# Kernel tuning notes

Hardware: AMD Instinct MI355X
Metric: run time of the kernel (lower is better)

Reference implementation:

```python
import jax, jax.numpy as jnp
import numpy as np

H, W, N = 1024, 2048, 1572864
NF, NP, NIN = 32, 3, 5


def _linear_init(key, fan_in, fan_out):
    kw, kb = jax.random.split(key)
    bound = 1.0 / np.sqrt(fan_in)
    w = jax.random.uniform(kw, (fan_in, fan_out), jnp.float32, -bound, bound)
    b = jax.random.uniform(kb, (fan_out,), jnp.float32, -bound, bound)
    return w, b


def setup_inputs() -> dict:
    key = jax.random.key(0)
    ks = jax.random.split(key, 8)
    # grid: sub-pixel source coordinates, (2, N), x-row then y-row
    gx = jax.random.uniform(ks[0], (1, N), jnp.float32) * (W - 1)
    gy = jax.random.uniform(ks[1], (1, N), jnp.float32) * (H - 1)
    grid = jnp.concatenate([gx, gy], axis=0)
    # yi: unique flat pixel indices (torch index-assign assumes no duplicates)
    yi = jax.random.permutation(ks[2], H * W)[:N].astype(jnp.int32)
    # m: near-identity homography so the projective denominator stays well-conditioned
    m = jnp.eye(3, dtype=jnp.float32) + 0.05 * jax.random.normal(ks[3], (3, 3), jnp.float32)
    W1, b1 = _linear_init(ks[4], NIN, NF)
    W2, b2 = _linear_init(ks[5], NF, NF)
    W3, b3 = _linear_init(ks[6], NF, NF)
    W4, b4 = _linear_init(ks[7], NF, NP)
    return {"grid": grid, "yi": yi, "m": m,
            "W1": W1, "b1": b1, "W2": W2, "b2": b2,
            "W3": W3, "b3": b3, "W4": W4, "b4": b4,
            "size_h": H, "size_w": W}


def _calc_dsda_projective(m, h, w):
    # Area scale (Jacobian determinant magnitude) of the homography m at each
    # output pixel: |det(m)| / |m20*x + m21*y + m22|^3, flattened row-major (H*W,)
    xs = jnp.arange(w, dtype=jnp.float32)
    ys = jnp.arange(h, dtype=jnp.float32)
    denom = m[2, 0] * xs[None, :] + m[2, 1] * ys[:, None] + m[2, 2]  # (H, W)
    det = jnp.linalg.det(m)
    return (jnp.abs(det) / (jnp.abs(denom) ** 3)).reshape(-1)


def reference(grid, yi, m, W1, b1, W2, b2, W3, b3, W4, b4, size_h, size_w):
    h, w = size_h, size_w
    # --- feature construction (torch.no_grad block) ---
    dsda = _calc_dsda_projective(m, h, w)[yi][:, None]          # (N, 1) gather
    g = grid.T                                                  # (N, 2)
    gf = jnp.floor(g)
    tl = g - gf                                                 # x-fx, y-fy
    br = 1.0 - tl                                               # fx+1-x, fy+1-y
    x = jax.lax.stop_gradient(jnp.concatenate([tl, br, dsda], axis=1))  # (N, 5)
    # --- tiny 4-layer MLP ---
    hdd = jax.nn.relu(x @ W1 + b1)
    hdd = jax.nn.relu(hdd @ W2 + b2)
    hdd = jax.nn.relu(hdd @ W3 + b3)
    logits = hdd @ W4 + b4                                      # (N, NP)
    wgt = jax.nn.softmax(logits, axis=1)
    # --- scatter back to spatial layout ---
    w_spatial = jnp.zeros((h * w, NP), dtype=wgt.dtype).at[yi].set(wgt)
    return w_spatial.reshape(1, 1, h, w, NP)
```

## Files before the change

kernel.cpp:

```cpp
#include <hip/hip_runtime.h>


#define W_IMG 2048
#define NF    32

typedef __attribute__((ext_vector_type(8))) _Float16 f16x8;
typedef __attribute__((ext_vector_type(4))) _Float16 f16x4;
typedef __attribute__((ext_vector_type(4))) float    f32x4;

__global__ __launch_bounds__(256) void fill_zero(float* __restrict__ out, int n) {
    int n4 = n >> 2;
    float4* o4 = (float4*)out;
    int stride = gridDim.x * blockDim.x;
    for (int i = blockIdx.x * blockDim.x + threadIdx.x; i < n4; i += stride)
        o4[i] = make_float4(0.f, 0.f, 0.f, 0.f);
    int t = (n4 << 2) + (blockIdx.x * blockDim.x + threadIdx.x);
    if (t < n) out[t] = 0.f;
}

__global__ __launch_bounds__(256, 4) void msampler_mlp(
    const float* __restrict__ grid,
    const int*   __restrict__ yi,
    const float* __restrict__ m,
    const float* __restrict__ W1, const float* __restrict__ b1,
    const float* __restrict__ W2, const float* __restrict__ b2,
    const float* __restrict__ W3, const float* __restrict__ b3,
    const float* __restrict__ W4, const float* __restrict__ b4,
    float* __restrict__ out, int N)
{
    const int tid  = threadIdx.x;
    const int lane = tid & 63;
    const int wave = tid >> 6;
    const int lm   = lane & 15;
    const int lq   = lane >> 4;

    __shared__ __align__(16) char smem[4 * 8192];
    char* buf = smem + wave * 8192;

    f16x8 a1[2], a2[2], a3[2], a4;
    f32x4 cb1[2], cb2[2], cb3[2], cb4;
#pragma unroll
    for (int mh = 0; mh < 2; ++mh) {
        int outc = 16 * mh + lm;
#pragma unroll
        for (int j = 0; j < 8; ++j) {
            int k = lq * 8 + j;
            a1[mh][j] = (k < 5) ? (_Float16)W1[k * NF + outc] : (_Float16)0.0f;
            a2[mh][j] = (_Float16)W2[k * NF + outc];
            a3[mh][j] = (_Float16)W3[k * NF + outc];
        }
#pragma unroll
        for (int r = 0; r < 4; ++r) {
            int o = 16 * mh + lq * 4 + r;
            cb1[mh][r] = b1[o];
            cb2[mh][r] = b2[o];
            cb3[mh][r] = b3[o];
        }
    }
#pragma unroll
    for (int j = 0; j < 8; ++j) {
        int k = lq * 8 + j;
        a4[j] = (lm < 3) ? (_Float16)W4[k * 3 + lm] : (_Float16)0.0f;
    }
#pragma unroll
    for (int r = 0; r < 4; ++r) {
        int o = lq * 4 + r;
        cb4[r] = (o < 3) ? b4[o] : 0.f;
    }

    float m00=m[0], m01=m[1], m02=m[2];
    float m10=m[3], m11=m[4], m12=m[5];
    float m20=m[6], m21=m[7], m22=m[8];
    float det = m00*(m11*m22 - m12*m21)
              - m01*(m10*m22 - m12*m20)
              + m02*(m10*m21 - m11*m20);
    float adet = fabsf(det);

    const int i0 = blockIdx.x * 512 + wave * 128;
    int ya[2];
#pragma unroll
    for (int t = 0; t < 2; ++t) {
        int i  = i0 + t * 64 + lane;
        int ic = i < N ? i : N - 1;
        float gx = grid[ic];
        float gy = grid[N + ic];
        int   y  = yi[ic];
        ya[t] = y;
        int py = y >> 11;
        int px = y & (W_IMG - 1);
        float denom = m20*(float)px + m21*(float)py + m22;
        float ad    = fabsf(denom);
        float dsda  = fminf(adet / (ad*ad*ad), 60000.f);
        float fx = gx - floorf(gx);
        float fy = gy - floorf(gy);
        f16x8 f;
        f[0] = (_Float16)fx;         f[1] = (_Float16)fy;
        f[2] = (_Float16)(1.f-fx);   f[3] = (_Float16)(1.f-fy);
        f[4] = (_Float16)dsda;       f[5] = (_Float16)0.0f;
        f[6] = (_Float16)0.0f;       f[7] = (_Float16)0.0f;
        int g = t * 4 + lq;
        *(f16x8*)(buf + g * 1024 + lm * 16) = f;
    }
    {
        f16x8 z = {};
#pragma unroll
        for (int j = 0; j < 6; ++j) {
            int T  = lane >> 3;
            int ch = (lane & 7) + 8 * j;
            *(f16x8*)(buf + T * 1024 + 256 + ch * 16) = z;
        }
    }

    const int woff = ((lq >> 1) * 16 + lm) * 16 + (lq & 1) * 8;

#define LAYER(AF, CB)                                                          \
    _Pragma("unroll")                                                          \
    for (int tg = 0; tg < 2; ++tg) {                                           \
        f16x8 bf[4];                                                           \
        _Pragma("unroll")                                                      \
        for (int q = 0; q < 4; ++q)                                            \
            bf[q] = *(const f16x8*)(buf + (tg*4 + q) * 1024 + lane * 16);      \
        _Pragma("unroll")                                                      \
        for (int q = 0; q < 4; ++q) {                                          \
            int T = tg * 4 + q;                                                \
            _Pragma("unroll")                                                  \
            for (int mh = 0; mh < 2; ++mh) {                                   \
                f32x4 d = __builtin_amdgcn_mfma_f32_16x16x32_f16(              \
                    AF[mh], bf[q], CB[mh], 0, 0, 0);                           \
                f16x4 o;                                                       \
                _Pragma("unroll")                                              \
                for (int r = 0; r < 4; ++r)                                    \
                    o[r] = (_Float16)fminf(fmaxf(d[r], 0.f), 60000.f);         \
                *(f16x4*)(buf + T * 1024 + mh * 512 + woff) = o;               \
            }                                                                  \
        }                                                                      \
    }

    LAYER(a1, cb1)
    LAYER(a2, cb2)
    LAYER(a3, cb3)
#undef LAYER

#pragma unroll
    for (int tg = 0; tg < 2; ++tg) {
        f16x8 bf[4];
#pragma unroll
        for (int q = 0; q < 4; ++q)
            bf[q] = *(const f16x8*)(buf + (tg*4 + q) * 1024 + lane * 16);
#pragma unroll
        for (int q = 0; q < 4; ++q) {
            int T = tg * 4 + q;
            f32x4 d = __builtin_amdgcn_mfma_f32_16x16x32_f16(a4, bf[q], cb4, 0, 0, 0);
            if (lq == 0)
                *(f32x4*)(buf + (T * 16 + lm) * 16) = d;
        }
    }

#pragma unroll
    for (int t = 0; t < 2; ++t) {
        int s = t * 64 + lane;
        f32x4 L = *(const f32x4*)(buf + s * 16);
        float l0 = L[0], l1 = L[1], l2 = L[2];
        float mx = fmaxf(l0, fmaxf(l1, l2));
        float e0 = __expf(l0 - mx), e1 = __expf(l1 - mx), e2 = __expf(l2 - mx);
        float inv = 1.f / (e0 + e1 + e2);
        int i = i0 + s;
        if (i < N) {
            int o = ya[t] * 3;
            out[o + 0] = e0 * inv;
            out[o + 1] = e1 * inv;
            out[o + 2] = e2 * inv;
        }
    }
}

extern "C" void kernel_launch(void* const* d_in, const int* in_sizes, int n_in,
                              void* d_out, int out_size, void* d_ws, size_t ws_size,
                              hipStream_t stream) {
    const float* grid = (const float*)d_in[0];
    const int*   yi   = (const int*)  d_in[1];
    const float* m    = (const float*)d_in[2];
    const float* W1   = (const float*)d_in[3];
    const float* b1   = (const float*)d_in[4];
    const float* W2   = (const float*)d_in[5];
    const float* b2   = (const float*)d_in[6];
    const float* W3   = (const float*)d_in[7];
    const float* b3   = (const float*)d_in[8];
    const float* W4   = (const float*)d_in[9];
    const float* b4   = (const float*)d_in[10];
    float* out = (float*)d_out;

    int N = in_sizes[1];

    fill_zero<<<1024, 256, 0, stream>>>(out, out_size);

    int grid_sz = (N + 511) / 512;
    msampler_mlp<<<grid_sz, 256, 0, stream>>>(
        grid, yi, m, W1, b1, W2, b2, W3, b3, W4, b4, out, N);
}
```

Measured before the change: 129.5 us.

## Process 16 tiles per wave with 128-thread blocks and packed f16 conversion

Restructures the MLP kernel so each wave handles 256 samples (16 MFMA tiles) instead of 128, using 2 waves per block. The first layer now reads inputs from registers with zeros for the padded K lanes instead of zero-filling shared memory. ReLU outputs are converted with packed cvt_pkrtz, and the zero-fill kernel launches more blocks. The intent is to cut per-sample overhead and instruction count, at the cost of higher register pressure from 16 live B fragments and possibly lower occupancy.

```diff
diff --git a/kernel.cpp b/kernel.cpp
--- a/kernel.cpp
+++ b/kernel.cpp
@@ -3,10 +3,14 @@
 
 #define W_IMG 2048
 #define NF    32
+#define TILES 16
 
 typedef __attribute__((ext_vector_type(8))) _Float16 f16x8;
 typedef __attribute__((ext_vector_type(4))) _Float16 f16x4;
+typedef __attribute__((ext_vector_type(2))) __fp16   h16x2;
 typedef __attribute__((ext_vector_type(4))) float    f32x4;
+
+union PkU { f16x4 v; h16x2 h[2]; };
 
 __global__ __launch_bounds__(256) void fill_zero(float* __restrict__ out, int n) {
     int n4 = n >> 2;
@@ -18,7 +22,7 @@
     if (t < n) out[t] = 0.f;
 }
 
-__global__ __launch_bounds__(256, 4) void msampler_mlp(
+__global__ __launch_bounds__(128) void msampler_mlp(
     const float* __restrict__ grid,
     const int*   __restrict__ yi,
     const float* __restrict__ m,
@@ -34,8 +38,8 @@
     const int lm   = lane & 15;
     const int lq   = lane >> 4;
 
-    __shared__ __align__(16) char smem[4 * 8192];
-    char* buf = smem + wave * 8192;
+    __shared__ __align__(16) char smem[2 * TILES * 1024];
+    char* buf = smem + wave * (TILES * 1024);
 
     f16x8 a1[2], a2[2], a3[2], a4;
     f32x4 cb1[2], cb2[2], cb3[2], cb4;
@@ -76,10 +80,10 @@
               + m02*(m10*m21 - m11*m20);
     float adet = fabsf(det);
 
-    const int i0 = blockIdx.x * 512 + wave * 128;
-    int ya[2];
-#pragma unroll
-    for (int t = 0; t < 2; ++t) {
+    const int i0 = blockIdx.x * 512 + wave * 256;
+    int ya[4];
+#pragma unroll
+    for (int t = 0; t < 4; ++t) {
         int i  = i0 + t * 64 + lane;
         int ic = i < N ? i : N - 1;
         float gx = grid[ic];
@@ -101,70 +105,85 @@
         int g = t * 4 + lq;
         *(f16x8*)(buf + g * 1024 + lm * 16) = f;
     }
+
+    const int woff = (lq >> 1) * 256 + lm * 16 + (lq & 1) * 8;
+
     {
-        f16x8 z = {};
-#pragma unroll
-        for (int j = 0; j < 6; ++j) {
-            int T  = lane >> 3;
-            int ch = (lane & 7) + 8 * j;
-            *(f16x8*)(buf + T * 1024 + 256 + ch * 16) = z;
-        }
-    }
-
-    const int woff = ((lq >> 1) * 16 + lm) * 16 + (lq & 1) * 8;
+        f16x8 bf[TILES];
+#pragma unroll
+        for (int g = 0; g < TILES; ++g) {
+            f16x8 z = {};
+            if (lq == 0) z = *(const f16x8*)(buf + g * 1024 + lm * 16);
+            bf[g] = z;
+        }
+#pragma unroll
+        for (int g = 0; g < TILES; ++g) {
+#pragma unroll
+            for (int mh = 0; mh < 2; ++mh) {
+                f32x4 d = __builtin_amdgcn_mfma_f32_16x16x32_f16(
+                    a1[mh], bf[g], cb1[mh], 0, 0, 0);
+                PkU u;
+                u.h[0] = __builtin_amdgcn_cvt_pkrtz(
+                    fminf(fmaxf(d[0], 0.f), 60000.f),
+                    fminf(fmaxf(d[1], 0.f), 60000.f));
+                u.h[1] = __builtin_amdgcn_cvt_pkrtz(
+                    fminf(fmaxf(d[2], 0.f), 60000.f),
+                    fminf(fmaxf(d[3], 0.f), 60000.f));
+                *(f16x4*)(buf + g * 1024 + mh * 512 + woff) = u.v;
+            }
+        }
+    }
 
 #define LAYER(AF, CB)                                                          \
-    _Pragma("unroll")                                                          \
-    for (int tg = 0; tg < 2; ++tg) {                                           \
-        f16x8 bf[4];                                                           \
+    {                                                                          \
+        f16x8 bf[TILES];                                                       \
         _Pragma("unroll")                                                      \
-        for (int q = 0; q < 4; ++q)                                            \
-            bf[q] = *(const f16x8*)(buf + (tg*4 + q) * 1024 + lane * 16);      \
+        for (int g = 0; g < TILES; ++g)                                        \
+            bf[g] = *(const f16x8*)(buf + g * 1024 + lane * 16);               \
         _Pragma("unroll")                                                      \
-        for (int q = 0; q < 4; ++q) {                                          \
-            int T = tg * 4 + q;                                                \
+        for (int g = 0; g < TILES; ++g) {                                      \
             _Pragma("unroll")                                                  \
             for (int mh = 0; mh < 2; ++mh) {                                   \
                 f32x4 d = __builtin_amdgcn_mfma_f32_16x16x32_f16(              \
-                    AF[mh], bf[q], CB[mh], 0, 0, 0);                           \
-                f16x4 o;                                                       \
-                _Pragma("unroll")                                              \
-                for (int r = 0; r < 4; ++r)                                    \
-                    o[r] = (_Float16)fminf(fmaxf(d[r], 0.f), 60000.f);         \
-                *(f16x4*)(buf + T * 1024 + mh * 512 + woff) = o;               \
+                    AF[mh], bf[g], CB[mh], 0, 0, 0);                           \
+                PkU u;                                                         \
+                u.h[0] = __builtin_amdgcn_cvt_pkrtz(                           \
+                    fminf(fmaxf(d[0], 0.f), 60000.f),                          \
+                    fminf(fmaxf(d[1], 0.f), 60000.f));                         \
+                u.h[1] = __builtin_amdgcn_cvt_pkrtz(                           \
+                    fminf(fmaxf(d[2], 0.f), 60000.f),                          \
+                    fminf(fmaxf(d[3], 0.f), 60000.f));                         \
+                *(f16x4*)(buf + g * 1024 + mh * 512 + woff) = u.v;             \
             }                                                                  \
         }                                                                      \
     }
 
-    LAYER(a1, cb1)
     LAYER(a2, cb2)
     LAYER(a3, cb3)
 #undef LAYER
 
-#pragma unroll
-    for (int tg = 0; tg < 2; ++tg) {
-        f16x8 bf[4];
-#pragma unroll
-        for (int q = 0; q < 4; ++q)
-            bf[q] = *(const f16x8*)(buf + (tg*4 + q) * 1024 + lane * 16);
-#pragma unroll
-        for (int q = 0; q < 4; ++q) {
-            int T = tg * 4 + q;
-            f32x4 d = __builtin_amdgcn_mfma_f32_16x16x32_f16(a4, bf[q], cb4, 0, 0, 0);
+    {
+        f16x8 bf[TILES];
+#pragma unroll
+        for (int g = 0; g < TILES; ++g)
+            bf[g] = *(const f16x8*)(buf + g * 1024 + lane * 16);
+#pragma unroll
+        for (int g = 0; g < TILES; ++g) {
+            f32x4 d = __builtin_amdgcn_mfma_f32_16x16x32_f16(a4, bf[g], cb4, 0, 0, 0);
             if (lq == 0)
-                *(f32x4*)(buf + (T * 16 + lm) * 16) = d;
-        }
-    }
-
-#pragma unroll
-    for (int t = 0; t < 2; ++t) {
-        int s = t * 64 + lane;
-        f32x4 L = *(const f32x4*)(buf + s * 16);
+                *(f32x4*)(buf + g * 1024 + lm * 16) = d;
+        }
+    }
+
+#pragma unroll
+    for (int t = 0; t < 4; ++t) {
+        int g = t * 4 + lq;
+        f32x4 L = *(const f32x4*)(buf + g * 1024 + lm * 16);
         float l0 = L[0], l1 = L[1], l2 = L[2];
         float mx = fmaxf(l0, fmaxf(l1, l2));
         float e0 = __expf(l0 - mx), e1 = __expf(l1 - mx), e2 = __expf(l2 - mx);
         float inv = 1.f / (e0 + e1 + e2);
-        int i = i0 + s;
+        int i = i0 + t * 64 + lane;
         if (i < N) {
             int o = ya[t] * 3;
             out[o + 0] = e0 * inv;
@@ -192,9 +211,9 @@
 
     int N = in_sizes[1];
 
-    fill_zero<<<1024, 256, 0, stream>>>(out, out_size);
+    fill_zero<<<2048, 256, 0, stream>>>(out, out_size);
 
     int grid_sz = (N + 511) / 512;
-    msampler_mlp<<<grid_sz, 256, 0, stream>>>(
+    msampler_mlp<<<grid_sz, 128, 0, stream>>>(
         grid, yi, m, W1, b1, W2, b2, W3, b3, W4, b4, out, N);
 }
```

New measurement: 143.3 us. +10.6%, slower.
